# Performance work log

Hardware: AMD Instinct MI355X
Metric: run time of the kernel (lower is better)

Reference implementation:

```python
import jax, jax.numpy as jnp
import numpy as np

NS, NV = 48, 10                    # scalar / vector multiplicities (cfg.ns, cfg.nv)
WN = NS * NS + NS * NV             # per-edge TP weight numel: paths 0e*0e->0e and 0e*1o->1o
OUT = NS + 3 * NV                  # out irreps 48x0e + 10x1o -> 78 dims
INV = float(1.0 / np.sqrt(NS))     # e3nn-style path normalization (fan_in = mul_in)
N_LIG, N_REC, N_ATOM = 2000, 2000, 15000
E_LL, E_RR, E_AA = 15000, 10000, 15000
E_LR, E_LA, E_AR = 5000, 8000, 8000


def setup_inputs() -> dict:
    key = jax.random.key(0)
    ks = jax.random.split(key, 40)
    f = lambda i, shape, s=1.0: jax.random.normal(ks[i], shape, dtype=jnp.float32) * s
    ii = lambda i, n, e: jax.random.randint(ks[i], (e,), 0, n, dtype=jnp.int32)
    w_s = (1.0 / (3 * NS)) ** 0.5
    return {
        'lig_x': f(0, (N_LIG, NS)), 'rec_x': f(1, (N_REC, NS)), 'atom_x': f(2, (N_ATOM, NS)),
        'll_attr': f(3, (E_LL, NS)), 'rr_attr': f(4, (E_RR, NS)), 'aa_attr': f(5, (E_AA, NS)),
        'lr_attr': f(6, (E_LR, NS)), 'la_attr': f(7, (E_LA, NS)), 'ar_attr': f(8, (E_AR, NS)),
        'll_sh': f(9, (E_LL, 9)), 'rr_sh': f(10, (E_RR, 9)), 'aa_sh': f(11, (E_AA, 9)),
        'lr_sh': f(12, (E_LR, 9)), 'la_sh': f(13, (E_LA, 9)), 'ar_sh': f(14, (E_AR, 9)),
        'mlp_w1': f(15, (9, 3 * NS, 3 * NS), w_s), 'mlp_b1': jnp.zeros((9, 3 * NS), jnp.float32),
        'mlp_w2': f(16, (9, 3 * NS, 3 * NS), w_s), 'mlp_b2': jnp.zeros((9, 3 * NS), jnp.float32),
        'mlp_w3': f(17, (9, 3 * NS, WN), w_s), 'mlp_b3': jnp.zeros((9, WN), jnp.float32),
        'll_src': ii(18, N_LIG, E_LL), 'll_dst': ii(19, N_LIG, E_LL),
        'rr_src': ii(20, N_REC, E_RR), 'rr_dst': ii(21, N_REC, E_RR),
        'aa_src': ii(22, N_ATOM, E_AA), 'aa_dst': ii(23, N_ATOM, E_AA),
        'lr_lig': ii(24, N_LIG, E_LR), 'lr_rec': ii(25, N_REC, E_LR),
        'la_lig': ii(26, N_LIG, E_LA), 'la_atom': ii(27, N_ATOM, E_LA),
        'ar_atom': ii(28, N_ATOM, E_AR), 'ar_rec': ii(29, N_REC, E_AR),
    }


def _tp_conv(src_x, dst_x, e_attr, e_sh, src_idx, dst_idx, n_dst, w1, b1, w2, b2, w3, b3):
    """FullyConnectedTensorProductConv: per-edge MLP -> TP weights, CG tensor
    product of gathered source features with edge SH, mean scatter to dst."""
    fs = src_x[src_idx]                                          # (E, ns) gather
    z = jnp.concatenate([e_attr, fs, dst_x[dst_idx]], axis=-1)
    h = jax.nn.relu(z @ w1 + b1)
    h = jax.nn.relu(h @ w2 + b2)
    w = h @ w3 + b3                                              # (E, WN) edge-conditioned TP weights
    w0 = w[:, : NS * NS].reshape(-1, NS, NS)                     # 0e x 0e -> 0e path
    wv = w[:, NS * NS :].reshape(-1, NS, NV)                     # 0e x 1o -> 1o path
    out0 = jnp.einsum('ei,eio->eo', fs, w0) * e_sh[:, :1] * INV  # (E, ns)
    outv = jnp.einsum('ei,eiv,em->evm', fs, wv, e_sh[:, 1:4]) * INV  # (E, nv, 3)
    msg = jnp.concatenate([out0, outv.reshape(-1, NV * 3)], axis=-1)
    agg = jax.ops.segment_sum(msg, dst_idx, num_segments=n_dst)
    deg = jax.ops.segment_sum(jnp.ones((msg.shape[0], 1), msg.dtype), dst_idx, num_segments=n_dst)
    return agg / jnp.maximum(deg, 1.0)                           # mean reduction


def reference(lig_x, rec_x, atom_x, ll_attr, rr_attr, aa_attr, lr_attr, la_attr, ar_attr,
              ll_sh, rr_sh, aa_sh, lr_sh, la_sh, ar_sh,
              mlp_w1, mlp_b1, mlp_w2, mlp_b2, mlp_w3, mlp_b3,
              ll_src, ll_dst, rr_src, rr_dst, aa_src, aa_dst,
              lr_lig, lr_rec, la_lig, la_atom, ar_atom, ar_rec):
    P = lambda c: (mlp_w1[c], mlp_b1[c], mlp_w2[c], mlp_b2[c], mlp_w3[c], mlp_b3[c])
    # one interaction layer = 9 structurally distinct convs (lig/rec/atom intra + 6 cross dirs)
    lig_u = (_tp_conv(lig_x, lig_x, ll_attr, ll_sh, ll_src, ll_dst, N_LIG, *P(0))
           + _tp_conv(rec_x, lig_x, lr_attr, lr_sh, lr_rec, lr_lig, N_LIG, *P(1))
           + _tp_conv(atom_x, lig_x, la_attr, la_sh, la_atom, la_lig, N_LIG, *P(2)))
    rec_u = (_tp_conv(lig_x, rec_x, lr_attr, lr_sh, lr_lig, lr_rec, N_REC, *P(3))
           + _tp_conv(rec_x, rec_x, rr_attr, rr_sh, rr_src, rr_dst, N_REC, *P(4))
           + _tp_conv(atom_x, rec_x, ar_attr, ar_sh, ar_atom, ar_rec, N_REC, *P(5)))
    atom_u = (_tp_conv(lig_x, atom_x, la_attr, la_sh, la_lig, la_atom, N_ATOM, *P(6))
            + _tp_conv(rec_x, atom_x, ar_attr, ar_sh, ar_rec, ar_atom, N_ATOM, *P(7))
            + _tp_conv(atom_x, atom_x, aa_attr, aa_sh, aa_src, aa_dst, N_ATOM, *P(8)))
    pad = lambda x: jnp.pad(x, ((0, 0), (0, OUT - NS)))          # residual: pad scalars to out irreps
    return jnp.concatenate([pad(lig_x) + lig_u, pad(rec_x) + rec_u, pad(atom_x) + atom_u], axis=0)
```

## Files before the change

### kernel.cpp

```cpp
#include <hip/hip_runtime.h>


namespace {

constexpr int NCONV = 9;
constexpr int ETOT  = 82000;
constexpr float INV = 0.14433756729740643f;

constexpr int EC[NCONV]     = {15000,5000,8000,5000,10000,8000,8000,8000,15000};
constexpr int NBLKC[NCONV]  = {118,40,63,40,79,63,63,63,118};
constexpr int EOFF[NCONV]   = {0,15000,20000,28000,33000,43000,51000,59000,67000};
constexpr int DEGOFF[NCONV] = {0,2000,4000,6000,8000,10000,12000,27000,42000};
constexpr int NBLK_TOT = 647;

typedef _Float16 f16;
typedef __attribute__((ext_vector_type(8))) _Float16 f16x8;
typedef __attribute__((ext_vector_type(4))) _Float16 f16x4;
typedef __attribute__((ext_vector_type(4))) float f32x4;

#define MFMA(a, b, c) __builtin_amdgcn_mfma_f32_16x16x32_f16((a), (b), (c), 0, 0, 0)

struct ConvPtrs {
  const float* src_x[NCONV];
  const float* dst_x[NCONV];
  const float* attr[NCONV];
  const float* sh[NCONV];
  const int*   sidx[NCONV];
  const int*   didx[NCONV];
};

}

__device__ __forceinline__ int xcd_remap(int bid) {
  const int xcd = bid & 7, slot = bid >> 3;
  return (xcd <= 6) ? (xcd * 81 + slot) : (567 + slot);
}

__device__ __forceinline__ int conv_decode(int bid, int& rem) {
  int c = 0; rem = bid;
  while (c < NCONV - 1 && rem >= NBLKC[c]) { rem -= NBLKC[c]; ++c; }
  return c;
}

__device__ __forceinline__ void gld_lds16(const void* g, void* l) {
  __builtin_amdgcn_global_load_lds(
      (const __attribute__((address_space(1))) void*)g,
      (__attribute__((address_space(3))) void*)l, 16, 0, 0);
}

__device__ __forceinline__ f32x4 cvt4(f16x4 h) {
  return (f32x4){(float)h[0], (float)h[1], (float)h[2], (float)h[3]};
}

__global__ __launch_bounds__(64) void prep_w12(
    const float* __restrict__ w1, const float* __restrict__ b1,
    const float* __restrict__ w2, const float* __restrict__ b2,
    f16* __restrict__ w1f, f16* __restrict__ w2f) {
  const int b = blockIdx.x;
  const int sel = b >= 405, bb = sel ? b - 405 : b;
  const int c = bb / 45, r2 = bb % 45, cb = r2 / 5, s = r2 % 5;
  const float* w  = sel ? w2 : w1;
  const float* bi = sel ? b2 : b1;
  f16* dst = (sel ? w2f : w1f) + ((size_t)(c * 9 + cb) * 5 + s) * 512;
  const int l = threadIdx.x;
  const int n = cb * 16 + (l & 15);
  f16x8 pack;
#pragma unroll
  for (int j = 0; j < 8; ++j) {
    const int k = s * 32 + ((l >> 4) << 3) + j;
    float v = 0.f;
    if (k < 144)       v = w[((size_t)c * 144 + k) * 144 + n];
    else if (k == 144) v = bi[c * 144 + n];
    pack[j] = (f16)v;
  }
  ((f16x8*)dst)[l] = pack;
}

__global__ __launch_bounds__(256) void prep_w3k(
    const float* __restrict__ w3, const float* __restrict__ b3,
    f16* __restrict__ w3f) {
  const int b = blockIdx.x;
  const int c = b / 48, i = b % 48;
  const float* wc = w3 + (size_t)c * 144 * 2784;
  const float* bc = b3 + (size_t)c * 2784;
  f16* dst = w3f + (size_t)(c * 48 + i) * 20 * 512;
#pragma unroll 1
  for (int it = 0; it < 40; ++it) {
    const int f = it * 256 + threadIdx.x;
    const int s = f >> 11, g2 = f & 2047, cb = g2 >> 9, l = (g2 >> 3) & 63, j = f & 7;
    const int k = s * 32 + ((l >> 4) << 3) + j;
    const int col = cb * 16 + (l & 15);
    float v = 0.f;
    if (k <= 144) {
      const float* src = (k == 144) ? bc : (wc + (size_t)k * 2784);
      if (col < 48)      v = src[i * 48 + col];
      else if (col < 58) v = src[2304 + i * 10 + (col - 48)];
    }
    dst[f] = (f16)v;
  }
}

__global__ __launch_bounds__(256) void deg_kernel(ConvPtrs P, float* __restrict__ deg) {
  const int gid = blockIdx.x * 256 + threadIdx.x;
  if (gid >= ETOT) return;
  int c = 0;
  while (c < NCONV - 1 && gid >= EOFF[c + 1]) ++c;
  const int e = gid - EOFF[c];
  atomicAdd(&deg[DEGOFF[c] + P.didx[c][e]], 1.0f);
}

__global__ __launch_bounds__(256) void resid_kernel(
    const float* __restrict__ lig, const float* __restrict__ rec,
    const float* __restrict__ atom, float* __restrict__ out) {
  const int gid = blockIdx.x * 256 + threadIdx.x;
  if (gid >= 19000 * 78) return;
  const int row = gid / 78, j = gid - row * 78;
  const float* x; int node;
  if (row < 2000)      { x = lig;  node = row; }
  else if (row < 4000) { x = rec;  node = row - 2000; }
  else                 { x = atom; node = row - 4000; }
  out[gid] = (j < 48) ? x[(size_t)node * 48 + j] : 0.f;
}

template<int NCB, int CB0>
__device__ __forceinline__ void layer_mm(
    const f16x8* __restrict__ Av, const f16x8* __restrict__ wv,
    int c, int lane, int wr, f32x4 acc[4][5]) {
#pragma unroll
  for (int rb = 0; rb < 4; ++rb)
#pragma unroll
    for (int cb = 0; cb < NCB; ++cb) acc[rb][cb] = (f32x4)0.0f;
#pragma unroll
  for (int s = 0; s < 5; ++s) {
    f16x8 B[NCB];
#pragma unroll
    for (int cb = 0; cb < NCB; ++cb)
      B[cb] = wv[((size_t)(c * 9 + CB0 + cb) * 5 + s) * 64 + lane];
    f16x8 A[4];
#pragma unroll
    for (int rb = 0; rb < 4; ++rb) A[rb] = Av[((wr * 4 + rb) * 5 + s) * 64 + lane];
#pragma unroll
    for (int rb = 0; rb < 4; ++rb)
#pragma unroll
      for (int cb = 0; cb < NCB; ++cb)
        acc[rb][cb] = MFMA(A[rb], B[cb], acc[rb][cb]);
  }
}

template<int NCB, int CB0>
__device__ __forceinline__ void layer_wb(const f32x4 acc[4][5], f16* __restrict__ At,
                                         int lane, int wr) {
#pragma unroll
  for (int cb = 0; cb < NCB; ++cb) {
    const int k = (CB0 + cb) * 16 + (lane & 15);
    const int s = k >> 5, g = (k >> 3) & 3, j = k & 7;
#pragma unroll
    for (int rb = 0; rb < 4; ++rb)
#pragma unroll
      for (int r = 0; r < 4; ++r) {
        const int row = ((lane >> 4) << 2) + r;
        At[((((wr * 4 + rb) * 5 + s) * 4 + g) * 16 + row) * 8 + j] =
            (f16)fmaxf(acc[rb][cb][r], 0.f);
      }
  }
}

__global__ __launch_bounds__(256, 3) void fused_conv(
    ConvPtrs P, const f16* __restrict__ w1f, const f16* __restrict__ w2f,
    const f16* __restrict__ w3f, const float* __restrict__ deg,
    float* __restrict__ out) {
  __shared__ __align__(16) char smem[54272];
  f16* Atile = (f16*)smem;
  f16 (*fst)[128] = (f16 (*)[128])(smem + 40960);
  int* sidb = (int*)(smem + 53248);
  int* dstb = (int*)(smem + 53760);

  int rem; const int c = conv_decode(xcd_remap(blockIdx.x), rem);
  const int E = EC[c], e0 = rem * 128;
  const int tid = threadIdx.x, lane = tid & 63, w = tid >> 6;
  const int wr = w >> 1, wc = w & 1;

  if (tid < 128) {
    int ec = e0 + tid; if (ec >= E) ec = E - 1;
    sidb[tid] = P.sidx[c][ec];
    dstb[tid] = P.didx[c][ec];
  }
  __syncthreads();

  {
    const float* attr = P.attr[c];
    const float* sx = P.src_x[c];
    const float* dx = P.dst_x[c];
#pragma unroll 1
    for (int it = 0; it < 10; ++it) {
      const int u = it * 256 + tid, j8 = u >> 7, e = u & 127;
      int ec = e0 + e; if (ec >= E) ec = E - 1;
      float v[8];
      if (j8 < 6) {
        const float* p = attr + (size_t)ec * 48 + j8 * 8;
#pragma unroll
        for (int t = 0; t < 8; ++t) v[t] = p[t];
      } else if (j8 < 12) {
        const float* p = sx + (size_t)sidb[e] * 48 + (j8 - 6) * 8;
#pragma unroll
        for (int t = 0; t < 8; ++t) v[t] = p[t];
#pragma unroll
        for (int t = 0; t < 8; ++t) fst[(j8 - 6) * 8 + t][e] = (f16)v[t];
      } else if (j8 < 18) {
        const float* p = dx + (size_t)dstb[e] * 48 + (j8 - 12) * 8;
#pragma unroll
        for (int t = 0; t < 8; ++t) v[t] = p[t];
      } else if (j8 == 18) {
        v[0] = 1.f;
#pragma unroll
        for (int t = 1; t < 8; ++t) v[t] = 0.f;
      } else {
#pragma unroll
        for (int t = 0; t < 8; ++t) v[t] = 0.f;
      }
      f16x8 h;
#pragma unroll
      for (int t = 0; t < 8; ++t) h[t] = (f16)v[t];
      const int s = j8 >> 2, g = j8 & 3, rbg = e >> 4, row = e & 15;
      ((f16x8*)Atile)[((rbg * 5 + s) * 4 + g) * 16 + row] = h;
    }
  }
  __syncthreads();

  const f16x8* Av = (const f16x8*)Atile;

  f32x4 acc[4][5];
  if (wc == 0) layer_mm<5, 0>(Av, (const f16x8*)w1f, c, lane, wr, acc);
  else         layer_mm<4, 5>(Av, (const f16x8*)w1f, c, lane, wr, acc);
  __syncthreads();
  if (wc == 0) layer_wb<5, 0>(acc, Atile, lane, wr);
  else         layer_wb<4, 5>(acc, Atile, lane, wr);
  __syncthreads();
  if (wc == 0) layer_mm<5, 0>(Av, (const f16x8*)w2f, c, lane, wr, acc);
  else         layer_mm<4, 5>(Av, (const f16x8*)w2f, c, lane, wr, acc);
  __syncthreads();
  if (wc == 0) layer_wb<5, 0>(acc, Atile, lane, wr);
  else         layer_wb<4, 5>(acc, Atile, lane, wr);
  __syncthreads();

  f16x8 Af[4][5];
#pragma unroll
  for (int rb = 0; rb < 4; ++rb)
#pragma unroll
    for (int s = 0; s < 5; ++s)
      Af[rb][s] = Av[((wr * 4 + rb) * 5 + s) * 64 + lane];
  __syncthreads();

  const f16* __restrict__ w3c = w3f + (size_t)(c * 48) * 10240;
  f16* buf0 = Atile;
  f16* buf1 = Atile + 10240;

  f32x4 msg[4][2];
#pragma unroll
  for (int rb = 0; rb < 4; ++rb)
#pragma unroll
    for (int cb = 0; cb < 2; ++cb) msg[rb][cb] = (f32x4)0.0f;

#pragma unroll
  for (int q = 0; q < 5; ++q) {
    const int chunk = q * 4 + w;
    gld_lds16(w3c + chunk * 512 + lane * 8, buf0 + chunk * 512);
  }
  __syncthreads();

#pragma unroll 1
  for (int i = 0; i < 48; ++i) {
    f16* bcur = (i & 1) ? buf1 : buf0;
    f16* bnxt = (i & 1) ? buf0 : buf1;
    if (i + 1 < 48) {
      const f16* gsrc = w3c + (size_t)(i + 1) * 10240;
#pragma unroll
      for (int q = 0; q < 5; ++q) {
        const int chunk = q * 4 + w;
        gld_lds16(gsrc + chunk * 512 + lane * 8, bnxt + chunk * 512);
      }
    }
    f16x4 fsh[4];
#pragma unroll
    for (int rb = 0; rb < 4; ++rb)
      fsh[rb] = *(const f16x4*)&fst[i][wr * 64 + rb * 16 + ((lane >> 4) << 2)];

    const f16x8* bv = (const f16x8*)bcur;
#pragma unroll
    for (int cb = 0; cb < 2; ++cb) {
      f16x8 Bf[5];
#pragma unroll
      for (int s = 0; s < 5; ++s) Bf[s] = bv[(s * 4 + wc * 2 + cb) * 64 + lane];
      f32x4 T[4];
#pragma unroll
      for (int rb = 0; rb < 4; ++rb) T[rb] = (f32x4)0.0f;
#pragma unroll
      for (int s = 0; s < 5; ++s)
#pragma unroll
        for (int rb = 0; rb < 4; ++rb) T[rb] = MFMA(Af[rb][s], Bf[s], T[rb]);
#pragma unroll
      for (int rb = 0; rb < 4; ++rb) msg[rb][cb] += cvt4(fsh[rb]) * T[rb];
    }
    __syncthreads();
  }

  const int outbase = (c < 3) ? 0 : (c < 6 ? 2000 : 4000);
  const float* __restrict__ shp = P.sh[c];
  const float* __restrict__ degc = deg + DEGOFF[c];
#pragma unroll
  for (int rb = 0; rb < 4; ++rb)
#pragma unroll
    for (int r = 0; r < 4; ++r) {
      const int el = wr * 64 + rb * 16 + ((lane >> 4) << 2) + r;
      const int ec = e0 + el;
      if (ec >= E) continue;
      const int dst = dstb[el];
      const float sc = INV / fmaxf(degc[dst], 1.f);
      const float* shq = shp + (size_t)ec * 9;
      const float s0 = shq[0], s1 = shq[1], s2 = shq[2], s3 = shq[3];
      float* op = out + ((size_t)outbase + dst) * 78;
#pragma unroll
      for (int cb = 0; cb < 2; ++cb) {
        const int col = (wc * 2 + cb) * 16 + (lane & 15);
        const float v = msg[rb][cb][r] * sc;
        if (col < 48) {
          atomicAdd(op + col, v * s0);
        } else if (col < 58) {
          const int vv = col - 48;
          atomicAdd(op + 48 + vv * 3 + 0, v * s1);
          atomicAdd(op + 48 + vv * 3 + 1, v * s2);
          atomicAdd(op + 48 + vv * 3 + 2, v * s3);
        }
      }
    }
}

extern "C" void kernel_launch(void* const* d_in, const int* in_sizes, int n_in,
                              void* d_out, int out_size, void* d_ws, size_t ws_size,
                              hipStream_t stream) {
  (void)in_sizes; (void)n_in; (void)out_size; (void)ws_size;
  const float* lig_x  = (const float*)d_in[0];
  const float* rec_x  = (const float*)d_in[1];
  const float* atom_x = (const float*)d_in[2];
  const float* attr_ll = (const float*)d_in[3];
  const float* attr_rr = (const float*)d_in[4];
  const float* attr_aa = (const float*)d_in[5];
  const float* attr_lr = (const float*)d_in[6];
  const float* attr_la = (const float*)d_in[7];
  const float* attr_ar = (const float*)d_in[8];
  const float* sh_ll = (const float*)d_in[9];
  const float* sh_rr = (const float*)d_in[10];
  const float* sh_aa = (const float*)d_in[11];
  const float* sh_lr = (const float*)d_in[12];
  const float* sh_la = (const float*)d_in[13];
  const float* sh_ar = (const float*)d_in[14];
  const float* w1 = (const float*)d_in[15];
  const float* b1 = (const float*)d_in[16];
  const float* w2 = (const float*)d_in[17];
  const float* b2 = (const float*)d_in[18];
  const float* w3 = (const float*)d_in[19];
  const float* b3 = (const float*)d_in[20];
  const int* ll_src = (const int*)d_in[21];
  const int* ll_dst = (const int*)d_in[22];
  const int* rr_src = (const int*)d_in[23];
  const int* rr_dst = (const int*)d_in[24];
  const int* aa_src = (const int*)d_in[25];
  const int* aa_dst = (const int*)d_in[26];
  const int* lr_lig = (const int*)d_in[27];
  const int* lr_rec = (const int*)d_in[28];
  const int* la_lig = (const int*)d_in[29];
  const int* la_atom = (const int*)d_in[30];
  const int* ar_atom = (const int*)d_in[31];
  const int* ar_rec  = (const int*)d_in[32];

  f16* w1f = (f16*)d_ws;
  f16* w2f = w1f + 207360;
  f16* w3f = w2f + 207360;
  float* deg = (float*)(w3f + 4423680);

  ConvPtrs P;
  const float* SX[NCONV] = {lig_x, rec_x, atom_x, lig_x, rec_x, atom_x, lig_x, rec_x, atom_x};
  const float* DX[NCONV] = {lig_x, lig_x, lig_x, rec_x, rec_x, rec_x, atom_x, atom_x, atom_x};
  const float* AT[NCONV] = {attr_ll, attr_lr, attr_la, attr_lr, attr_rr, attr_ar, attr_la, attr_ar, attr_aa};
  const float* SH[NCONV] = {sh_ll, sh_lr, sh_la, sh_lr, sh_rr, sh_ar, sh_la, sh_ar, sh_aa};
  const int*   SI[NCONV] = {ll_src, lr_rec, la_atom, lr_lig, rr_src, ar_atom, la_lig, ar_rec, aa_src};
  const int*   DI[NCONV] = {ll_dst, lr_lig, la_lig, lr_rec, rr_dst, ar_rec, la_atom, ar_atom, aa_dst};
  for (int cc = 0; cc < NCONV; ++cc) {
    P.src_x[cc] = SX[cc]; P.dst_x[cc] = DX[cc]; P.attr[cc] = AT[cc];
    P.sh[cc] = SH[cc]; P.sidx[cc] = SI[cc]; P.didx[cc] = DI[cc];
  }

  prep_w12<<<810, 64, 0, stream>>>(w1, b1, w2, b2, w1f, w2f);
  prep_w3k<<<432, 256, 0, stream>>>(w3, b3, w3f);
  hipMemsetAsync(deg, 0, 57000 * sizeof(float), stream);
  deg_kernel<<<(ETOT + 255) / 256, 256, 0, stream>>>(P, deg);
  resid_kernel<<<(19000 * 78 + 255) / 256, 256, 0, stream>>>(lig_x, rec_x, atom_x, (float*)d_out);
  fused_conv<<<NBLK_TOT, 256, 0, stream>>>(P, w1f, w2f, w3f, deg, (float*)d_out);
}
```

Before: 205.6 us.

## Replace atomic scatter with CSR-sorted per-edge messages and gather finalize

The per-edge atomicAdd scatter into the output is replaced by writing each edge's 78-dim message to a workspace buffer. A CSR index is built per conv (prefix scan over degrees plus a slot kernel), and a finalize kernel gathers each node's incoming messages, applies the mean and adds the residual. This removes atomic contention on the output but adds two launches, a single-thread serial scan and extra global traffic for the message buffer. Within each node, slot order comes from atomic cursors, so summation order is nondeterministic.

```diff
diff --git a/kernel.cpp b/kernel.cpp
--- a/kernel.cpp
+++ b/kernel.cpp
@@ -11,6 +11,7 @@
 constexpr int NBLKC[NCONV]  = {118,40,63,40,79,63,63,63,118};
 constexpr int EOFF[NCONV]   = {0,15000,20000,28000,33000,43000,51000,59000,67000};
 constexpr int DEGOFF[NCONV] = {0,2000,4000,6000,8000,10000,12000,27000,42000};
+constexpr int NODEC[NCONV]  = {2000,2000,2000,2000,2000,2000,15000,15000,15000};
 constexpr int NBLK_TOT = 647;
 
 typedef _Float16 f16;
@@ -109,17 +110,40 @@
   atomicAdd(&deg[DEGOFF[c] + P.didx[c][e]], 1.0f);
 }
 
-__global__ __launch_bounds__(256) void resid_kernel(
-    const float* __restrict__ lig, const float* __restrict__ rec,
-    const float* __restrict__ atom, float* __restrict__ out) {
+__global__ __launch_bounds__(256) void scan_kernel(
+    const float* __restrict__ deg, int* __restrict__ offs, int* __restrict__ cursor) {
+  __shared__ int part[256];
+  const int c = blockIdx.x, N = NODEC[c], base = DEGOFF[c];
+  const int tid = threadIdx.x;
+  const int chunk = (N + 255) / 256;
+  const int start = tid * chunk;
+  const int end = (start + chunk < N) ? (start + chunk) : N;
+  int s = 0;
+  for (int i = start; i < end; ++i) s += (int)deg[base + i];
+  part[tid] = s;
+  __syncthreads();
+  if (tid == 0) {
+    int acc = 0;
+    for (int k = 0; k < 256; ++k) { int t = part[k]; part[k] = acc; acc += t; }
+  }
+  __syncthreads();
+  int acc = part[tid];
+  for (int i = start; i < end; ++i) {
+    offs[base + i] = acc; cursor[base + i] = acc;
+    acc += (int)deg[base + i];
+  }
+}
+
+__global__ __launch_bounds__(256) void slot_kernel(
+    ConvPtrs P, int* __restrict__ cursor, int* __restrict__ eslot) {
   const int gid = blockIdx.x * 256 + threadIdx.x;
-  if (gid >= 19000 * 78) return;
-  const int row = gid / 78, j = gid - row * 78;
-  const float* x; int node;
-  if (row < 2000)      { x = lig;  node = row; }
-  else if (row < 4000) { x = rec;  node = row - 2000; }
-  else                 { x = atom; node = row - 4000; }
-  out[gid] = (j < 48) ? x[(size_t)node * 48 + j] : 0.f;
+  if (gid >= ETOT) return;
+  int c = 0;
+  while (c < NCONV - 1 && gid >= EOFF[c + 1]) ++c;
+  const int e = gid - EOFF[c];
+  const int d = P.didx[c][e];
+  const int pos = atomicAdd(&cursor[DEGOFF[c] + d], 1);
+  eslot[EOFF[c] + pos] = e;
 }
 
 template<int NCB, int CB0>
@@ -167,8 +191,7 @@
 
 __global__ __launch_bounds__(256, 3) void fused_conv(
     ConvPtrs P, const f16* __restrict__ w1f, const f16* __restrict__ w2f,
-    const f16* __restrict__ w3f, const float* __restrict__ deg,
-    float* __restrict__ out) {
+    const f16* __restrict__ w3f, float* __restrict__ medge) {
   __shared__ __align__(16) char smem[54272];
   f16* Atile = (f16*)smem;
   f16 (*fst)[128] = (f16 (*)[128])(smem + 40960);
@@ -304,9 +327,7 @@
     __syncthreads();
   }
 
-  const int outbase = (c < 3) ? 0 : (c < 6 ? 2000 : 4000);
   const float* __restrict__ shp = P.sh[c];
-  const float* __restrict__ degc = deg + DEGOFF[c];
 #pragma unroll
   for (int rb = 0; rb < 4; ++rb)
 #pragma unroll
@@ -314,25 +335,55 @@
       const int el = wr * 64 + rb * 16 + ((lane >> 4) << 2) + r;
       const int ec = e0 + el;
       if (ec >= E) continue;
-      const int dst = dstb[el];
-      const float sc = INV / fmaxf(degc[dst], 1.f);
+      const size_t ge = (size_t)(EOFF[c] + ec);
       const float* shq = shp + (size_t)ec * 9;
       const float s0 = shq[0], s1 = shq[1], s2 = shq[2], s3 = shq[3];
-      float* op = out + ((size_t)outbase + dst) * 78;
+      float* mp = medge + ge * 80;
 #pragma unroll
       for (int cb = 0; cb < 2; ++cb) {
         const int col = (wc * 2 + cb) * 16 + (lane & 15);
-        const float v = msg[rb][cb][r] * sc;
+        const float v = msg[rb][cb][r] * INV;
         if (col < 48) {
-          atomicAdd(op + col, v * s0);
+          mp[col] = v * s0;
         } else if (col < 58) {
           const int vv = col - 48;
-          atomicAdd(op + 48 + vv * 3 + 0, v * s1);
-          atomicAdd(op + 48 + vv * 3 + 1, v * s2);
-          atomicAdd(op + 48 + vv * 3 + 2, v * s3);
+          mp[48 + vv * 3 + 0] = v * s1;
+          mp[48 + vv * 3 + 1] = v * s2;
+          mp[48 + vv * 3 + 2] = v * s3;
         }
       }
     }
+}
+
+__global__ __launch_bounds__(256) void finalize_kernel(
+    const float* __restrict__ lig, const float* __restrict__ rec,
+    const float* __restrict__ atom, const float* __restrict__ deg,
+    const int* __restrict__ offs, const int* __restrict__ eslot,
+    const float* __restrict__ medge, float* __restrict__ out) {
+  const int half = threadIdx.x >> 7;
+  const int j = threadIdx.x & 127;
+  const int row = blockIdx.x * 2 + half;
+  if (row >= 19000 || j >= 78) return;
+  int node, cb; const float* x;
+  if (row < 2000)      { node = row;        cb = 0; x = lig; }
+  else if (row < 4000) { node = row - 2000; cb = 3; x = rec; }
+  else                 { node = row - 4000; cb = 6; x = atom; }
+  float r = (j < 48) ? x[(size_t)node * 48 + j] : 0.f;
+#pragma unroll
+  for (int t = 0; t < 3; ++t) {
+    const int c = cb + t;
+    const int base = DEGOFF[c] + node;
+    const float d = deg[base];
+    const int n = (int)d;
+    const int o = offs[base];
+    float s = 0.f;
+    for (int k = 0; k < n; ++k) {
+      const int e = eslot[EOFF[c] + o + k];
+      s += medge[(size_t)(EOFF[c] + e) * 80 + j];
+    }
+    r += s * (1.f / fmaxf(d, 1.f));
+  }
+  out[(size_t)row * 78 + j] = r;
 }
 
 extern "C" void kernel_launch(void* const* d_in, const int* in_sizes, int n_in,
@@ -376,7 +427,11 @@
   f16* w1f = (f16*)d_ws;
   f16* w2f = w1f + 207360;
   f16* w3f = w2f + 207360;
-  float* deg = (float*)(w3f + 4423680);
+  float* deg   = (float*)(w3f + 4423680);
+  int*   offs  = (int*)(deg + 57000);
+  int*   cursor= offs + 57000;
+  int*   eslot = cursor + 57000;
+  float* medge = (float*)(eslot + 82000);
 
   ConvPtrs P;
   const float* SX[NCONV] = {lig_x, rec_x, atom_x, lig_x, rec_x, atom_x, lig_x, rec_x, atom_x};
@@ -394,6 +449,9 @@
   prep_w3k<<<432, 256, 0, stream>>>(w3, b3, w3f);
   hipMemsetAsync(deg, 0, 57000 * sizeof(float), stream);
   deg_kernel<<<(ETOT + 255) / 256, 256, 0, stream>>>(P, deg);
-  resid_kernel<<<(19000 * 78 + 255) / 256, 256, 0, stream>>>(lig_x, rec_x, atom_x, (float*)d_out);
-  fused_conv<<<NBLK_TOT, 256, 0, stream>>>(P, w1f, w2f, w3f, deg, (float*)d_out);
-}
+  scan_kernel<<<NCONV, 256, 0, stream>>>(deg, offs, cursor);
+  slot_kernel<<<(ETOT + 255) / 256, 256, 0, stream>>>(P, cursor, eslot);
+  fused_conv<<<NBLK_TOT, 256, 0, stream>>>(P, w1f, w2f, w3f, medge);
+  finalize_kernel<<<9500, 256, 0, stream>>>(lig_x, rec_x, atom_x, deg, offs,
+                                            eslot, medge, (float*)d_out);
+}
```

After: 231.9 us. 12.8% more time.
